# Kernel tuning notes

Hardware: AMD Instinct MI355X
Metric: run time of the kernel (lower is better)

The kernel has to match this reference:

```python
import jax, jax.numpy as jnp
import numpy as np

SEQ, BATCH, HID, LAYERS = 512, 64, 1024, 2
SCALE = 0.02  # keep tanh out of full saturation for weight init


def setup_inputs() -> dict:
    key = jax.random.key(0)
    ks = jax.random.split(key, 6)
    return {
        "x": jax.random.normal(ks[0], (SEQ, BATCH, HID), dtype=jnp.float32),
        "h0": jax.random.normal(ks[1], (LAYERS, BATCH, HID), dtype=jnp.float32),
        "Wx": jax.random.normal(ks[2], (LAYERS, HID, HID), dtype=jnp.float32) * SCALE,
        "bx": jax.random.normal(ks[3], (LAYERS, HID), dtype=jnp.float32) * SCALE,
        "Wh": jax.random.normal(ks[4], (LAYERS, HID, HID), dtype=jnp.float32) * SCALE,
        "bh": jax.random.normal(ks[5], (LAYERS, HID), dtype=jnp.float32) * SCALE,
    }


def reference(x, h0, Wx, bx, Wh, bh):
    # x: [T, B, H]; h0: [L, B, H]; Wx/Wh: [L, H, H]; bx/bh: [L, H]
    num_layers = h0.shape[0]

    def step(h, x_t):
        # h: [L, B, H]; x_t: [B, H]
        inp = x_t
        new_h = []
        for l in range(num_layers):
            igate = inp @ Wx[l].T + bx[l]
            hgate = h[l] @ Wh[l].T + bh[l]
            h_l = jnp.tanh(igate + hgate)
            new_h.append(h_l)
            inp = h_l
        h_next = jnp.stack(new_h)
        return h_next, 10.0 * h_next[-1]

    h_n, output = jax.lax.scan(step, h0, x)
    return output, h_n
```

## Files before the change

kernel.cpp:

```cpp
#include <hip/hip_runtime.h>
#include <cstddef>
#include <cstdint>

#define HID     1024
#define BATCH   64
#define TSEQ    512
#define NB      (BATCH*HID)
#define NBLK    256
#define NITER   515
#define RSTRIDE 20


typedef __attribute__((ext_vector_type(4))) float f32x4;
typedef __attribute__((ext_vector_type(2))) float f32x2;

#define WAITV(N) do { asm volatile("s_waitcnt vmcnt(" #N ")" ::: "memory"); \
                      __builtin_amdgcn_sched_barrier(0); } while (0)

__device__ __forceinline__ f32x4 gload4(const float* p) {
  f32x4 v;
  asm volatile("global_load_dwordx4 %0, %1, off" : "=v"(v) : "v"(p) : "memory");
  return v;
}

__device__ __forceinline__ f32x2 gload2(const float* p) {
  f32x2 v;
  asm volatile("global_load_dwordx2 %0, %1, off" : "=v"(v) : "v"(p) : "memory");
  return v;
}

__device__ __forceinline__ void gstore2_coh(float* p, f32x2 v) {
  asm volatile("global_store_dwordx2 %0, %1, off sc1" :: "v"(p), "v"(v) : "memory");
}

__device__ __forceinline__ void gbar(unsigned* bar, unsigned target) {
  asm volatile("s_waitcnt vmcnt(0)" ::: "memory");
  __syncthreads();
  if (threadIdx.x == 0) {
    __hip_atomic_fetch_add(bar, 1u, __ATOMIC_RELAXED, __HIP_MEMORY_SCOPE_AGENT);
    while (__hip_atomic_load(bar, __ATOMIC_RELAXED, __HIP_MEMORY_SCOPE_AGENT) < target) {
      __builtin_amdgcn_s_sleep(1);
    }
  }
  __syncthreads();
}

__device__ __forceinline__ void fma16(f32x2 acc[16], const f32x4 h[8], const float* Wc) {
#pragma unroll 4
  for (int c = 0; c < 16; ++c) {
    const float* w = Wc + (size_t)c * HID;
    f32x2 s = acc[c];
#pragma unroll
    for (int r = 0; r < 8; ++r) {
      float4 wv = *(const float4*)(w + r * 4);
      f32x2 h01; h01.x = h[r].x; h01.y = h[r].y;
      f32x2 h23; h23.x = h[r].z; h23.y = h[r].w;
      f32x2 w01; w01.x = wv.x; w01.y = wv.y;
      f32x2 w23; w23.x = wv.z; w23.y = wv.w;
      s += h01 * w01;
      s += h23 * w23;
    }
    acc[c] = s;
  }
}

__device__ __forceinline__ void dot_engine(const float* hb, const float* Wb, f32x2 acc[16]) {
  f32x4 A[8], B[8];
#pragma unroll
  for (int r = 0; r < 8; ++r) A[r] = gload4(hb + r * 4);
#pragma unroll
  for (int r = 0; r < 8; ++r) B[r] = gload4(hb + 32 + r * 4);
  WAITV(8);
  fma16(acc, A, Wb);
#pragma unroll
  for (int r = 0; r < 8; ++r) A[r] = gload4(hb + 64 + r * 4);
  WAITV(8);
  fma16(acc, B, Wb + 32);
#pragma unroll
  for (int r = 0; r < 8; ++r) B[r] = gload4(hb + 96 + r * 4);
  WAITV(8);
  fma16(acc, A, Wb + 64);
  WAITV(0);
  fma16(acc, B, Wb + 96);
}

__global__ __launch_bounds__(512, 2) void rnn_step(
    const float* __restrict__ x,
    float* io,
    const float* __restrict__ h0_init,
    const float* __restrict__ Wx,
    const float* __restrict__ Wh,
    const float* __restrict__ bx,
    const float* __restrict__ bh,
    float* __restrict__ ws,
    unsigned P, unsigned mask)
{
  __shared__ __align__(16) float red[8 * 64 * RSTRIDE];
  const int tid  = threadIdx.x;
  const int blk  = blockIdx.x;
  const int role = blk >> 6;
  const int c0   = (blk & 63) << 4;
  const int b    = tid & 63;
  const int kq   = __builtin_amdgcn_readfirstlane(tid >> 6);

  float* h0base = ws;
  float* h1base = ws + (size_t)P * NB;
  float* igbase = ws + (size_t)2 * P * NB;
  unsigned* bar = (unsigned*)(ws + (size_t)3 * P * NB);

  const float* W = (role == 3) ? Wx
                 : (role == 0) ? Wh
                 : (role == 1) ? (Wx + (size_t)HID * HID)
                 :               (Wh + (size_t)HID * HID);
  const float* Wb = W + (size_t)c0 * HID + kq * 128;

  const int o0 = tid * 2;
  const int b1 = o0 >> 4;
  const int c1 = o0 & 15;
  const size_t rb = (size_t)b1 * HID + c0 + c1;

  float bsum0 = 0.f, bsum1 = 0.f;
  if (role == 1) {
    bsum0 = bx[HID + c0 + c1]     + bh[HID + c0 + c1];
    bsum1 = bx[HID + c0 + c1 + 1] + bh[HID + c0 + c1 + 1];
  } else if (role == 3) {
    bsum0 = bx[c0 + c1]     + bh[c0 + c1];
    bsum1 = bx[c0 + c1 + 1] + bh[c0 + c1 + 1];
  }

  for (int i = 0; i < NITER; ++i) {
    if ((i & (int)mask) == 0 && i) {
      __builtin_amdgcn_fence(__ATOMIC_ACQUIRE, "agent");
    }

    bool active;
    int t;
    const float* src;
    if (role == 3)      { t = i;     active = (i <= 511);           src = x + (size_t)t * NB; }
    else if (role == 0) { t = i - 1; active = (i >= 1 && i <= 512);
                          src = (t == 0) ? h0_init : h0base + (size_t)((t - 1) & mask) * NB; }
    else if (role == 1) { t = i - 2; active = (i >= 2 && i <= 513);
                          src = h0base + (size_t)(t & mask) * NB; }
    else                { t = i - 3; active = (i >= 3 && i <= 514);
                          src = (t == 0) ? (h0_init + NB) : h1base + (size_t)((t - 1) & mask) * NB; }

    if (active) {
      f32x2 e = { 0.f, 0.f };
      if (role == 0)      e = gload2(io + (size_t)t * NB + rb);
      else if (role == 2) e = gload2(igbase + (size_t)(t & mask) * NB + rb);

      const float* hb = src + (size_t)b * HID + kq * 128;

      f32x2 acc[16];
#pragma unroll
      for (int c = 0; c < 16; ++c) acc[c] = f32x2{0.f, 0.f};

      dot_engine(hb, Wb, acc);

      float accs[16];
#pragma unroll
      for (int c = 0; c < 16; ++c) accs[c] = acc[c].x + acc[c].y;

      float* rrow = &red[(kq * 64 + b) * RSTRIDE];
      *(float4*)(rrow + 0)  = make_float4(accs[0],  accs[1],  accs[2],  accs[3]);
      *(float4*)(rrow + 4)  = make_float4(accs[4],  accs[5],  accs[6],  accs[7]);
      *(float4*)(rrow + 8)  = make_float4(accs[8],  accs[9],  accs[10], accs[11]);
      *(float4*)(rrow + 12) = make_float4(accs[12], accs[13], accs[14], accs[15]);
      __syncthreads();

      float s0 = 0.f, s1 = 0.f;
#pragma unroll
      for (int q = 0; q < 8; ++q) {
        s0 += red[(q * 64 + b1) * RSTRIDE + c1];
        s1 += red[(q * 64 + b1) * RSTRIDE + c1 + 1];
      }

      if (role == 3) {
        f32x2 o = { s0 + bsum0, s1 + bsum1 };
        gstore2_coh(io + (size_t)t * NB + rb, o);
      } else if (role == 0) {
        f32x2 o = { tanhf(s0 + e.x), tanhf(s1 + e.y) };
        gstore2_coh(h0base + (size_t)(t & mask) * NB + rb, o);
      } else if (role == 1) {
        f32x2 o = { s0 + bsum0, s1 + bsum1 };
        gstore2_coh(igbase + (size_t)(t & mask) * NB + rb, o);
      } else {
        float t0 = tanhf(s0 + e.x);
        float t1 = tanhf(s1 + e.y);
        f32x2 o = { t0, t1 };
        gstore2_coh(h1base + (size_t)(t & mask) * NB + rb, o);
        *(float2*)&io[(size_t)t * NB + rb] = make_float2(10.f * t0, 10.f * t1);
      }
    }
    gbar(bar, (unsigned)(NBLK * (i + 1)));
  }
}

__global__ __launch_bounds__(256) void finalize_hn(
    const float* __restrict__ ws, float* __restrict__ out, unsigned P, unsigned mask)
{
  const int g = blockIdx.x * 256 + threadIdx.x;
  const float* h0f = ws + (size_t)(511u & mask) * NB;
  const float* h1f = ws + (size_t)(P + (511u & mask)) * NB;
  const float v = (g < NB) ? h0f[g] : h1f[g - NB];
  out[(size_t)TSEQ * NB + g] = v;
}

extern "C" void kernel_launch(void* const* d_in, const int* in_sizes, int n_in,
                              void* d_out, int out_size, void* d_ws, size_t ws_size,
                              hipStream_t stream) {
  const float* x  = (const float*)d_in[0];
  const float* h0 = (const float*)d_in[1];
  const float* Wx = (const float*)d_in[2];
  const float* bx = (const float*)d_in[3];
  const float* Wh = (const float*)d_in[4];
  const float* bh = (const float*)d_in[5];
  float* out = (float*)d_out;
  float* ws  = (float*)d_ws;

  unsigned P = 16;
  while (P > 2 && ((size_t)3 * P * NB + 16) * sizeof(float) > ws_size) P >>= 1;
  unsigned mask = P - 1;

  hipMemsetAsync(ws + (size_t)3 * P * NB, 0, sizeof(unsigned), stream);

  float* io = out;
  void* args[] = { &x, &io, &h0, &Wx, &Wh, &bx, &bh, &ws, &P, &mask };
  hipLaunchCooperativeKernel((const void*)rnn_step, dim3(NBLK), dim3(512),
                             args, 0, stream);

  finalize_hn<<<dim3(512), dim3(256), 0, stream>>>(ws, out, P, mask);
}
```

Before: 19.35 ms.

## Stage hidden-state chunks through LDS with coalesced double-buffered loads

Each thread used to load its own batch row's 128-wide K slice straight from global memory, which is uncoalesced across lanes. Now the block loads 128-column chunks of all 64 batch rows with coalesced float4 loads into a padded LDS buffer, double-buffered in registers, and each warp reads its 16-wide K slice from LDS. The K split across warps becomes interleaved in groups of 16 per chunk, and launch bounds are raised to 4 blocks per SM. In exchange it adds two __syncthreads per chunk (16 per step) and about 33KB of extra LDS.

Measured after the change: 37.49 ms. +93.8%, slower.

```diff
diff --git a/kernel.cpp b/kernel.cpp
--- a/kernel.cpp
+++ b/kernel.cpp
@@ -9,25 +9,10 @@
 #define NBLK    256
 #define NITER   515
 #define RSTRIDE 20
-
-
-typedef __attribute__((ext_vector_type(4))) float f32x4;
+#define HSTRIDE 129
+
+
 typedef __attribute__((ext_vector_type(2))) float f32x2;
-
-#define WAITV(N) do { asm volatile("s_waitcnt vmcnt(" #N ")" ::: "memory"); \
-                      __builtin_amdgcn_sched_barrier(0); } while (0)
-
-__device__ __forceinline__ f32x4 gload4(const float* p) {
-  f32x4 v;
-  asm volatile("global_load_dwordx4 %0, %1, off" : "=v"(v) : "v"(p) : "memory");
-  return v;
-}
-
-__device__ __forceinline__ f32x2 gload2(const float* p) {
-  f32x2 v;
-  asm volatile("global_load_dwordx2 %0, %1, off" : "=v"(v) : "v"(p) : "memory");
-  return v;
-}
 
 __device__ __forceinline__ void gstore2_coh(float* p, f32x2 v) {
   asm volatile("global_store_dwordx2 %0, %1, off sc1" :: "v"(p), "v"(v) : "memory");
@@ -45,46 +30,7 @@
   __syncthreads();
 }
 
-__device__ __forceinline__ void fma16(f32x2 acc[16], const f32x4 h[8], const float* Wc) {
-#pragma unroll 4
-  for (int c = 0; c < 16; ++c) {
-    const float* w = Wc + (size_t)c * HID;
-    f32x2 s = acc[c];
-#pragma unroll
-    for (int r = 0; r < 8; ++r) {
-      float4 wv = *(const float4*)(w + r * 4);
-      f32x2 h01; h01.x = h[r].x; h01.y = h[r].y;
-      f32x2 h23; h23.x = h[r].z; h23.y = h[r].w;
-      f32x2 w01; w01.x = wv.x; w01.y = wv.y;
-      f32x2 w23; w23.x = wv.z; w23.y = wv.w;
-      s += h01 * w01;
-      s += h23 * w23;
-    }
-    acc[c] = s;
-  }
-}
-
-__device__ __forceinline__ void dot_engine(const float* hb, const float* Wb, f32x2 acc[16]) {
-  f32x4 A[8], B[8];
-#pragma unroll
-  for (int r = 0; r < 8; ++r) A[r] = gload4(hb + r * 4);
-#pragma unroll
-  for (int r = 0; r < 8; ++r) B[r] = gload4(hb + 32 + r * 4);
-  WAITV(8);
-  fma16(acc, A, Wb);
-#pragma unroll
-  for (int r = 0; r < 8; ++r) A[r] = gload4(hb + 64 + r * 4);
-  WAITV(8);
-  fma16(acc, B, Wb + 32);
-#pragma unroll
-  for (int r = 0; r < 8; ++r) B[r] = gload4(hb + 96 + r * 4);
-  WAITV(8);
-  fma16(acc, A, Wb + 64);
-  WAITV(0);
-  fma16(acc, B, Wb + 96);
-}
-
-__global__ __launch_bounds__(512, 2) void rnn_step(
+__global__ __launch_bounds__(512, 4) void rnn_step(
     const float* __restrict__ x,
     float* io,
     const float* __restrict__ h0_init,
@@ -96,6 +42,7 @@
     unsigned P, unsigned mask)
 {
   __shared__ __align__(16) float red[8 * 64 * RSTRIDE];
+  __shared__ __align__(16) float hbuf[64 * HSTRIDE];
   const int tid  = threadIdx.x;
   const int blk  = blockIdx.x;
   const int role = blk >> 6;
@@ -103,6 +50,9 @@
   const int b    = tid & 63;
   const int kq   = __builtin_amdgcn_readfirstlane(tid >> 6);
 
+  const int srow = tid >> 5;
+  const int skol = (tid & 31) << 2;
+
   float* h0base = ws;
   float* h1base = ws + (size_t)P * NB;
   float* igbase = ws + (size_t)2 * P * NB;
@@ -112,7 +62,7 @@
                  : (role == 0) ? Wh
                  : (role == 1) ? (Wx + (size_t)HID * HID)
                  :               (Wh + (size_t)HID * HID);
-  const float* Wb = W + (size_t)c0 * HID + kq * 128;
+  const float* Wb = W + (size_t)c0 * HID + kq * 16;
 
   const int o0 = tid * 2;
   const int b1 = o0 >> 4;
@@ -145,17 +95,63 @@
                           src = (t == 0) ? (h0_init + NB) : h1base + (size_t)((t - 1) & mask) * NB; }
 
     if (active) {
-      f32x2 e = { 0.f, 0.f };
-      if (role == 0)      e = gload2(io + (size_t)t * NB + rb);
-      else if (role == 2) e = gload2(igbase + (size_t)(t & mask) * NB + rb);
-
-      const float* hb = src + (size_t)b * HID + kq * 128;
+      float e0 = 0.f, e1 = 0.f;
+      if (role == 0)      { e0 = io[(size_t)t * NB + rb];
+                            e1 = io[(size_t)t * NB + rb + 1]; }
+      else if (role == 2) { const float* ig = igbase + (size_t)(t & mask) * NB;
+                            e0 = ig[rb]; e1 = ig[rb + 1]; }
 
       f32x2 acc[16];
 #pragma unroll
       for (int c = 0; c < 16; ++c) acc[c] = f32x2{0.f, 0.f};
 
-      dot_engine(hb, Wb, acc);
+      float4 stA[4], stB[4];
+#pragma unroll
+      for (int r = 0; r < 4; ++r)
+        stA[r] = *(const float4*)(src + (size_t)(r * 16 + srow) * HID + skol);
+
+#pragma unroll 1
+      for (int cc = 0; cc < 8; ++cc) {
+        __syncthreads();
+        const float4* stw = (cc & 1) ? stB : stA;
+#pragma unroll
+        for (int r = 0; r < 4; ++r)
+          *(float4*)&hbuf[(r * 16 + srow) * HSTRIDE + skol] = stw[r];
+        if (cc < 7) {
+          float4* stn = (cc & 1) ? stA : stB;
+#pragma unroll
+          for (int r = 0; r < 4; ++r)
+            stn[r] = *(const float4*)(src + (size_t)(r * 16 + srow) * HID
+                                      + (cc + 1) * 128 + skol);
+        }
+        __syncthreads();
+
+        const float* hr = &hbuf[b * HSTRIDE + kq * 16];
+        float4 h0v = *(const float4*)(hr + 0);
+        float4 h1v = *(const float4*)(hr + 4);
+        float4 h2v = *(const float4*)(hr + 8);
+        float4 h3v = *(const float4*)(hr + 12);
+
+        const float* Wc = Wb + cc * 128;
+#pragma unroll 4
+        for (int c = 0; c < 16; ++c) {
+          const float* w = Wc + (size_t)c * HID;
+          float4 w0 = *(const float4*)(w + 0);
+          float4 w1 = *(const float4*)(w + 4);
+          float4 w2 = *(const float4*)(w + 8);
+          float4 w3 = *(const float4*)(w + 12);
+          f32x2 s = acc[c];
+          s += f32x2{h0v.x, h0v.y} * f32x2{w0.x, w0.y};
+          s += f32x2{h0v.z, h0v.w} * f32x2{w0.z, w0.w};
+          s += f32x2{h1v.x, h1v.y} * f32x2{w1.x, w1.y};
+          s += f32x2{h1v.z, h1v.w} * f32x2{w1.z, w1.w};
+          s += f32x2{h2v.x, h2v.y} * f32x2{w2.x, w2.y};
+          s += f32x2{h2v.z, h2v.w} * f32x2{w2.z, w2.w};
+          s += f32x2{h3v.x, h3v.y} * f32x2{w3.x, w3.y};
+          s += f32x2{h3v.z, h3v.w} * f32x2{w3.z, w3.w};
+          acc[c] = s;
+        }
+      }
 
       float accs[16];
 #pragma unroll
@@ -179,14 +175,14 @@
         f32x2 o = { s0 + bsum0, s1 + bsum1 };
         gstore2_coh(io + (size_t)t * NB + rb, o);
       } else if (role == 0) {
-        f32x2 o = { tanhf(s0 + e.x), tanhf(s1 + e.y) };
+        f32x2 o = { tanhf(s0 + e0), tanhf(s1 + e1) };
         gstore2_coh(h0base + (size_t)(t & mask) * NB + rb, o);
       } else if (role == 1) {
         f32x2 o = { s0 + bsum0, s1 + bsum1 };
         gstore2_coh(igbase + (size_t)(t & mask) * NB + rb, o);
       } else {
-        float t0 = tanhf(s0 + e.x);
-        float t1 = tanhf(s1 + e.y);
+        float t0 = tanhf(s0 + e0);
+        float t1 = tanhf(s1 + e1);
         f32x2 o = { t0, t1 };
         gstore2_coh(h1base + (size_t)(t & mask) * NB + rb, o);
         *(float2*)&io[(size_t)t * NB + rb] = make_float2(10.f * t0, 10.f * t1);
```

## Store hidden-state ring buffers transposed (k-major) for coalesced recurrent loads

Applied to the files above, without the earlier changes.

Hidden-state and gate intermediates in the workspace move to a [k][batch] transposed layout. Each lane now reads single dwords that are coalesced across the batch lanes, replacing the strided per-batch float4 rows. A small init kernel transposes h0 into the ring-buffer slot, and finalize un-transposes the last states. The cost is 16-deep scalar load batches, more instructions per FMA group, and strided scalar stores for the final output.

New measurement: 17.85 ms. 7.8% less time.

```diff
diff --git a/kernel.cpp b/kernel.cpp
--- a/kernel.cpp
+++ b/kernel.cpp
@@ -23,9 +23,9 @@
   return v;
 }
 
-__device__ __forceinline__ f32x2 gload2(const float* p) {
-  f32x2 v;
-  asm volatile("global_load_dwordx2 %0, %1, off" : "=v"(v) : "v"(p) : "memory");
+__device__ __forceinline__ float gload1(const float* p) {
+  float v;
+  asm volatile("global_load_dword %0, %1, off" : "=v"(v) : "v"(p) : "memory");
   return v;
 }
 
@@ -45,7 +45,54 @@
   __syncthreads();
 }
 
-__device__ __forceinline__ void fma16(f32x2 acc[16], const f32x4 h[8], const float* Wc) {
+__device__ __forceinline__ void load16(float (&A)[16], const float* hTb, int k0) {
+#pragma unroll
+  for (int j = 0; j < 16; ++j) A[j] = gload1(hTb + (size_t)(k0 + j) * 64);
+}
+
+__device__ __forceinline__ void fma16t(f32x2 (&acc)[16], const float (&h)[16], const float* Wc) {
+#pragma unroll 4
+  for (int c = 0; c < 16; ++c) {
+    const float* w = Wc + (size_t)c * HID;
+    float4 w0 = *(const float4*)(w + 0);
+    float4 w1 = *(const float4*)(w + 4);
+    float4 w2 = *(const float4*)(w + 8);
+    float4 w3 = *(const float4*)(w + 12);
+    f32x2 s = acc[c];
+    s += f32x2{h[0],  h[1]}  * f32x2{w0.x, w0.y};
+    s += f32x2{h[2],  h[3]}  * f32x2{w0.z, w0.w};
+    s += f32x2{h[4],  h[5]}  * f32x2{w1.x, w1.y};
+    s += f32x2{h[6],  h[7]}  * f32x2{w1.z, w1.w};
+    s += f32x2{h[8],  h[9]}  * f32x2{w2.x, w2.y};
+    s += f32x2{h[10], h[11]} * f32x2{w2.z, w2.w};
+    s += f32x2{h[12], h[13]} * f32x2{w3.x, w3.y};
+    s += f32x2{h[14], h[15]} * f32x2{w3.z, w3.w};
+    acc[c] = s;
+  }
+}
+
+__device__ __forceinline__ void dot_engine_T(const float* hTb, const float* Wb,
+                                             int k0, f32x2 (&acc)[16]) {
+  float A[16], B[16];
+  load16(A, hTb, k0);
+  load16(B, hTb, k0 + 16);
+  WAITV(16); fma16t(acc, A, Wb);
+  load16(A, hTb, k0 + 32);
+  WAITV(16); fma16t(acc, B, Wb + 16);
+  load16(B, hTb, k0 + 48);
+  WAITV(16); fma16t(acc, A, Wb + 32);
+  load16(A, hTb, k0 + 64);
+  WAITV(16); fma16t(acc, B, Wb + 48);
+  load16(B, hTb, k0 + 80);
+  WAITV(16); fma16t(acc, A, Wb + 64);
+  load16(A, hTb, k0 + 96);
+  WAITV(16); fma16t(acc, B, Wb + 80);
+  load16(B, hTb, k0 + 112);
+  WAITV(16); fma16t(acc, A, Wb + 96);
+  WAITV(0);  fma16t(acc, B, Wb + 112);
+}
+
+__device__ __forceinline__ void fma16x4(f32x2 (&acc)[16], const f32x4 (&h)[8], const float* Wc) {
 #pragma unroll 4
   for (int c = 0; c < 16; ++c) {
     const float* w = Wc + (size_t)c * HID;
@@ -53,41 +100,45 @@
 #pragma unroll
     for (int r = 0; r < 8; ++r) {
       float4 wv = *(const float4*)(w + r * 4);
-      f32x2 h01; h01.x = h[r].x; h01.y = h[r].y;
-      f32x2 h23; h23.x = h[r].z; h23.y = h[r].w;
-      f32x2 w01; w01.x = wv.x; w01.y = wv.y;
-      f32x2 w23; w23.x = wv.z; w23.y = wv.w;
-      s += h01 * w01;
-      s += h23 * w23;
+      s += f32x2{h[r].x, h[r].y} * f32x2{wv.x, wv.y};
+      s += f32x2{h[r].z, h[r].w} * f32x2{wv.z, wv.w};
     }
     acc[c] = s;
   }
 }
 
-__device__ __forceinline__ void dot_engine(const float* hb, const float* Wb, f32x2 acc[16]) {
+__device__ __forceinline__ void dot_engine_x(const float* hb, const float* Wb, f32x2 (&acc)[16]) {
   f32x4 A[8], B[8];
 #pragma unroll
   for (int r = 0; r < 8; ++r) A[r] = gload4(hb + r * 4);
 #pragma unroll
   for (int r = 0; r < 8; ++r) B[r] = gload4(hb + 32 + r * 4);
-  WAITV(8);
-  fma16(acc, A, Wb);
+  WAITV(8); fma16x4(acc, A, Wb);
 #pragma unroll
   for (int r = 0; r < 8; ++r) A[r] = gload4(hb + 64 + r * 4);
-  WAITV(8);
-  fma16(acc, B, Wb + 32);
+  WAITV(8); fma16x4(acc, B, Wb + 32);
 #pragma unroll
   for (int r = 0; r < 8; ++r) B[r] = gload4(hb + 96 + r * 4);
-  WAITV(8);
-  fma16(acc, A, Wb + 64);
-  WAITV(0);
-  fma16(acc, B, Wb + 96);
+  WAITV(8); fma16x4(acc, A, Wb + 64);
+  WAITV(0); fma16x4(acc, B, Wb + 96);
+}
+
+__global__ __launch_bounds__(256) void init_hT(
+    const float* __restrict__ h0_init, float* __restrict__ ws,
+    unsigned P, unsigned mask)
+{
+  const int g = blockIdx.x * 256 + threadIdx.x;
+  const int l = g >> 16;
+  const int r = g & 65535;
+  const int k = r >> 6;
+  const int b = r & 63;
+  float* base = ws + (size_t)l * P * NB + (size_t)mask * NB;
+  base[r] = h0_init[(size_t)l * NB + (size_t)b * HID + k];
 }
 
 __global__ __launch_bounds__(512, 2) void rnn_step(
     const float* __restrict__ x,
     float* io,
-    const float* __restrict__ h0_init,
     const float* __restrict__ Wx,
     const float* __restrict__ Wh,
     const float* __restrict__ bx,
@@ -102,6 +153,7 @@
   const int c0   = (blk & 63) << 4;
   const int b    = tid & 63;
   const int kq   = __builtin_amdgcn_readfirstlane(tid >> 6);
+  const int k0   = kq * 128;
 
   float* h0base = ws;
   float* h1base = ws + (size_t)P * NB;
@@ -112,21 +164,15 @@
                  : (role == 0) ? Wh
                  : (role == 1) ? (Wx + (size_t)HID * HID)
                  :               (Wh + (size_t)HID * HID);
-  const float* Wb = W + (size_t)c0 * HID + kq * 128;
-
-  const int o0 = tid * 2;
-  const int b1 = o0 >> 4;
-  const int c1 = o0 & 15;
-  const size_t rb = (size_t)b1 * HID + c0 + c1;
-
-  float bsum0 = 0.f, bsum1 = 0.f;
-  if (role == 1) {
-    bsum0 = bx[HID + c0 + c1]     + bh[HID + c0 + c1];
-    bsum1 = bx[HID + c0 + c1 + 1] + bh[HID + c0 + c1 + 1];
-  } else if (role == 3) {
-    bsum0 = bx[c0 + c1]     + bh[c0 + c1];
-    bsum1 = bx[c0 + c1 + 1] + bh[c0 + c1 + 1];
-  }
+  const float* Wb = W + (size_t)c0 * HID + k0;
+
+  const int cE = tid >> 5;
+  const int bE = (tid & 31) << 1;
+  const size_t rbT = (size_t)(c0 + cE) * 64 + bE;
+
+  float bsum = 0.f;
+  if (role == 1)      bsum = bx[HID + c0 + cE] + bh[HID + c0 + cE];
+  else if (role == 3) bsum = bx[c0 + cE]       + bh[c0 + cE];
 
   for (int i = 0; i < NITER; ++i) {
     if ((i & (int)mask) == 0 && i) {
@@ -138,24 +184,23 @@
     const float* src;
     if (role == 3)      { t = i;     active = (i <= 511);           src = x + (size_t)t * NB; }
     else if (role == 0) { t = i - 1; active = (i >= 1 && i <= 512);
-                          src = (t == 0) ? h0_init : h0base + (size_t)((t - 1) & mask) * NB; }
+                          src = h0base + (size_t)((t - 1) & (int)mask) * NB; }
     else if (role == 1) { t = i - 2; active = (i >= 2 && i <= 513);
-                          src = h0base + (size_t)(t & mask) * NB; }
+                          src = h0base + (size_t)(t & (int)mask) * NB; }
     else                { t = i - 3; active = (i >= 3 && i <= 514);
-                          src = (t == 0) ? (h0_init + NB) : h1base + (size_t)((t - 1) & mask) * NB; }
+                          src = h1base + (size_t)((t - 1) & (int)mask) * NB; }
 
     if (active) {
+      f32x2 acc[16];
+#pragma unroll
+      for (int c = 0; c < 16; ++c) acc[c] = f32x2{0.f, 0.f};
+
+      if (role == 3) dot_engine_x(src + (size_t)b * HID + k0, Wb, acc);
+      else           dot_engine_T(src + b, Wb, k0, acc);
+
       f32x2 e = { 0.f, 0.f };
-      if (role == 0)      e = gload2(io + (size_t)t * NB + rb);
-      else if (role == 2) e = gload2(igbase + (size_t)(t & mask) * NB + rb);
-
-      const float* hb = src + (size_t)b * HID + kq * 128;
-
-      f32x2 acc[16];
-#pragma unroll
-      for (int c = 0; c < 16; ++c) acc[c] = f32x2{0.f, 0.f};
-
-      dot_engine(hb, Wb, acc);
+      if (role == 0)      e = *(const f32x2*)(io + (size_t)t * NB + rbT);
+      else if (role == 2) e = *(const f32x2*)(igbase + (size_t)(t & (int)mask) * NB + rbT);
 
       float accs[16];
 #pragma unroll
@@ -171,25 +216,24 @@
       float s0 = 0.f, s1 = 0.f;
 #pragma unroll
       for (int q = 0; q < 8; ++q) {
-        s0 += red[(q * 64 + b1) * RSTRIDE + c1];
-        s1 += red[(q * 64 + b1) * RSTRIDE + c1 + 1];
+        s0 += red[(q * 64 + bE)     * RSTRIDE + cE];
+        s1 += red[(q * 64 + bE + 1) * RSTRIDE + cE];
       }
 
       if (role == 3) {
-        f32x2 o = { s0 + bsum0, s1 + bsum1 };
-        gstore2_coh(io + (size_t)t * NB + rb, o);
+        gstore2_coh(io + (size_t)t * NB + rbT, f32x2{ s0 + bsum, s1 + bsum });
       } else if (role == 0) {
-        f32x2 o = { tanhf(s0 + e.x), tanhf(s1 + e.y) };
-        gstore2_coh(h0base + (size_t)(t & mask) * NB + rb, o);
+        gstore2_coh(h0base + (size_t)(t & (int)mask) * NB + rbT,
+                    f32x2{ tanhf(s0 + e.x), tanhf(s1 + e.y) });
       } else if (role == 1) {
-        f32x2 o = { s0 + bsum0, s1 + bsum1 };
-        gstore2_coh(igbase + (size_t)(t & mask) * NB + rb, o);
+        gstore2_coh(igbase + (size_t)(t & (int)mask) * NB + rbT,
+                    f32x2{ s0 + bsum, s1 + bsum });
       } else {
         float t0 = tanhf(s0 + e.x);
         float t1 = tanhf(s1 + e.y);
-        f32x2 o = { t0, t1 };
-        gstore2_coh(h1base + (size_t)(t & mask) * NB + rb, o);
-        *(float2*)&io[(size_t)t * NB + rb] = make_float2(10.f * t0, 10.f * t1);
+        gstore2_coh(h1base + (size_t)(t & (int)mask) * NB + rbT, f32x2{ t0, t1 });
+        io[(size_t)t * NB + (size_t)bE       * HID + c0 + cE] = 10.f * t0;
+        io[(size_t)t * NB + (size_t)(bE + 1) * HID + c0 + cE] = 10.f * t1;
       }
     }
     gbar(bar, (unsigned)(NBLK * (i + 1)));
@@ -200,10 +244,12 @@
     const float* __restrict__ ws, float* __restrict__ out, unsigned P, unsigned mask)
 {
   const int g = blockIdx.x * 256 + threadIdx.x;
-  const float* h0f = ws + (size_t)(511u & mask) * NB;
-  const float* h1f = ws + (size_t)(P + (511u & mask)) * NB;
-  const float v = (g < NB) ? h0f[g] : h1f[g - NB];
-  out[(size_t)TSEQ * NB + g] = v;
+  const int l = g >> 16;
+  const int rem = g & 65535;
+  const int bb = rem >> 10;
+  const int kk = rem & 1023;
+  const float* hf = ws + ((size_t)l * P + (511u & mask)) * NB;
+  out[(size_t)TSEQ * NB + g] = hf[(size_t)kk * 64 + bb];
 }
 
 extern "C" void kernel_launch(void* const* d_in, const int* in_sizes, int n_in,
@@ -223,9 +269,10 @@
   unsigned mask = P - 1;
 
   hipMemsetAsync(ws + (size_t)3 * P * NB, 0, sizeof(unsigned), stream);
+  init_hT<<<dim3(512), dim3(256), 0, stream>>>(h0, ws, P, mask);
 
   float* io = out;
-  void* args[] = { &x, &io, &h0, &Wx, &Wh, &bx, &bh, &ws, &P, &mask };
+  void* args[] = { &x, &io, &Wx, &Wh, &bx, &bh, &ws, &P, &mask };
   hipLaunchCooperativeKernel((const void*)rnn_step, dim3(NBLK), dim3(512),
                              args, 0, stream);
 
```
